# Kernel tuning notes

Hardware: AMD Instinct MI355X
Metric: run time of the kernel (lower is better)

Reference implementation:

```python
import jax, jax.numpy as jnp
import numpy as np

T, B, E, H = 2048, 2, 1024, 16
HD = E // H
EPS = 1e-5


def setup_inputs() -> dict:
    key = jax.random.key(0)
    k1, k2, k3 = jax.random.split(key, 3)
    bound_in = float(np.sqrt(6.0 / (3 * E + E)))   # xavier_uniform for [3E,E]
    bound_out = float(np.sqrt(6.0 / (E + E)))      # xavier_uniform for [E,E]
    return {
        "query": jax.random.normal(k1, (T, B, E), dtype=jnp.float32),
        "gamma": jnp.ones((E,), dtype=jnp.float32),
        "beta": jnp.zeros((E,), dtype=jnp.float32),
        "in_proj_weight": jax.random.uniform(k2, (3 * E, E), jnp.float32, -bound_in, bound_in),
        "out_proj_weight": jax.random.uniform(k3, (E, E), jnp.float32, -bound_out, bound_out),
    }


def reference(query, gamma, beta, in_proj_weight, out_proj_weight):
    # LayerNorm over channel dim
    mean = jnp.mean(query, axis=-1, keepdims=True)
    var = jnp.mean(jnp.square(query - mean), axis=-1, keepdims=True)
    ln = (query - mean) * jax.lax.rsqrt(var + EPS) * gamma + beta  # [T,B,E]

    # Fused QKV projection (no bias): qkv = ln @ W^T, W: [3E, E]
    qkv = jnp.einsum("tbe,fe->tbf", ln, in_proj_weight)  # [T,B,3E]
    q, k, v = jnp.split(qkv, 3, axis=-1)
    q = q.reshape(T, B, H, HD) * (HD ** -0.5)
    k = k.reshape(T, B, H, HD)
    v = v.reshape(T, B, H, HD)

    # Attention: scores [B,H,T,T]
    scores = jnp.einsum("tbhd,sbhd->bhts", q, k)
    attn = jax.nn.softmax(scores, axis=-1)
    ctx = jnp.einsum("bhts,sbhd->tbhd", attn, v).reshape(T, B, E)

    # Output projection + residual add (dropout prob = 0)
    out = jnp.einsum("tbe,fe->tbf", ctx, out_proj_weight)
    return query + out
```

## Files before the change

kernel.cpp:

```cpp
#include <hip/hip_runtime.h>
#include <hip/hip_bf16.h>
#include <math.h>

#define T_DIM 2048
#define B_DIM 2
#define E_DIM 1024
#define H_DIM 16
#define HD_DIM 64
#define M_DIM (T_DIM * B_DIM)
#define BH_DIM (B_DIM * H_DIM)

using bf16x8 = __attribute__((ext_vector_type(8))) __bf16;
using u16x8  = __attribute__((ext_vector_type(8))) unsigned short;
using u16x4  = __attribute__((ext_vector_type(4))) unsigned short;
using f32x4  = __attribute__((ext_vector_type(4))) float;

static __device__ __forceinline__ unsigned short f2bf(float f) {
  unsigned u = __builtin_bit_cast(unsigned, f);
  u += 0x7fff + ((u >> 16) & 1);
  return (unsigned short)(u >> 16);
}

__device__ __forceinline__ void gload_lds16(const void* g, void* l) {
  __builtin_amdgcn_global_load_lds(
      (const __attribute__((address_space(1))) unsigned int*)g,
      (__attribute__((address_space(3))) unsigned int*)l, 16, 0, 0);
}

__global__ __launch_bounds__(256) void cast_bf16_kernel(
    const float* __restrict__ in, unsigned short* __restrict__ out, int n4) {
  int i = blockIdx.x * 256 + threadIdx.x;
  if (i >= n4) return;
  float4 v = ((const float4*)in)[i];
  ushort4 o;
  o.x = f2bf(v.x); o.y = f2bf(v.y); o.z = f2bf(v.z); o.w = f2bf(v.w);
  ((ushort4*)out)[i] = o;
}

__global__ __launch_bounds__(256) void ln_kernel(
    const float* __restrict__ q, const float* __restrict__ gamma,
    const float* __restrict__ beta, unsigned short* __restrict__ out) {
  int row = blockIdx.x;
  int tid = threadIdx.x;
  const float4* qr = (const float4*)(q + (size_t)row * E_DIM);
  float4 x = qr[tid];
  float s  = x.x + x.y + x.z + x.w;
  float ss = x.x * x.x + x.y * x.y + x.z * x.z + x.w * x.w;
#pragma unroll
  for (int off = 32; off >= 1; off >>= 1) {
    s  += __shfl_xor(s, off, 64);
    ss += __shfl_xor(ss, off, 64);
  }
  __shared__ float red[8];
  int wid = tid >> 6, lane = tid & 63;
  if (lane == 0) { red[wid] = s; red[4 + wid] = ss; }
  __syncthreads();
  s  = red[0] + red[1] + red[2] + red[3];
  ss = red[4] + red[5] + red[6] + red[7];
  float mean = s * (1.0f / E_DIM);
  float var  = ss * (1.0f / E_DIM) - mean * mean;
  float rstd = rsqrtf(var + 1e-5f);
  float4 g4 = ((const float4*)gamma)[tid];
  float4 b4 = ((const float4*)beta)[tid];
  ushort4 o;
  o.x = f2bf((x.x - mean) * rstd * g4.x + b4.x);
  o.y = f2bf((x.y - mean) * rstd * g4.y + b4.y);
  o.z = f2bf((x.z - mean) * rstd * g4.z + b4.z);
  o.w = f2bf((x.w - mean) * rstd * g4.w + b4.w);
  ((ushort4*)(out + (size_t)row * E_DIM))[tid] = o;
}

template <int MODE>
__global__ __launch_bounds__(256) void gemm_bt_kernel(
    const unsigned short* __restrict__ A, const unsigned short* __restrict__ Bw,
    const float* __restrict__ resid, unsigned short* __restrict__ out_qkv,
    float* __restrict__ out_f, int Kv, int Nv) {
  __shared__ alignas(16) unsigned short lA[128 * 32];
  __shared__ alignas(16) unsigned short lB[128 * 32];
  int tid = threadIdx.x;
  int wid = tid >> 6, lane = tid & 63;
  int wm = wid >> 1, wn = wid & 1;
  int g = lane >> 4, lr = lane & 15;
  int m0 = blockIdx.y * 128, n0 = blockIdx.x * 128;
  f32x4 acc[4][4] = {};

  for (int k0 = 0; k0 < Kv; k0 += 32) {
#pragma unroll
    for (int c = 0; c < 2; ++c) {
      int f16 = c * 256 + tid;
      int row = f16 >> 2, col8 = (f16 & 3) << 3;
      gload_lds16(A  + (size_t)(m0 + row) * Kv + k0 + col8,
                  lA + (size_t)(c * 256 + wid * 64) * 8);
      gload_lds16(Bw + (size_t)(n0 + row) * Kv + k0 + col8,
                  lB + (size_t)(c * 256 + wid * 64) * 8);
    }
    __syncthreads();
    bf16x8 af[4], bfr[4];
#pragma unroll
    for (int r = 0; r < 4; ++r) {
      af[r]  = *(const bf16x8*)(lA + (wm * 64 + r * 16 + lr) * 32 + g * 8);
      bfr[r] = *(const bf16x8*)(lB + (wn * 64 + r * 16 + lr) * 32 + g * 8);
    }
#pragma unroll
    for (int mr = 0; mr < 4; ++mr)
#pragma unroll
      for (int nr = 0; nr < 4; ++nr)
        acc[mr][nr] = __builtin_amdgcn_mfma_f32_16x16x32_bf16(
            af[mr], bfr[nr], acc[mr][nr], 0, 0, 0);
    __syncthreads();
  }

#pragma unroll
  for (int mr = 0; mr < 4; ++mr) {
#pragma unroll
    for (int nr = 0; nr < 4; ++nr) {
#pragma unroll
      for (int r = 0; r < 4; ++r) {
        int grow = m0 + wm * 64 + mr * 16 + g * 4 + r;
        int gcol = n0 + wn * 64 + nr * 16 + lr;
        float v = acc[mr][nr][r];
        if (MODE == 0) {
          int which = gcol >> 10, rem = gcol & 1023;
          int h = rem >> 6, d = rem & 63;
          int t = grow >> 1, b = grow & 1;
          out_qkv[(size_t)which * (BH_DIM * T_DIM * HD_DIM) +
                  ((size_t)(b * H_DIM + h) * T_DIM + t) * HD_DIM + d] = f2bf(v);
        } else {
          size_t idx = (size_t)grow * Nv + gcol;
          out_f[idx] = resid[idx] + v;
        }
      }
    }
  }
}

__global__ __launch_bounds__(256) void transpose_v_kernel(
    const unsigned short* __restrict__ vb, unsigned short* __restrict__ vt) {
  __shared__ alignas(16) unsigned short tl[64 * 72];
  int tid = threadIdx.x;
  int bh = blockIdx.y, t0 = blockIdx.x * 64;
  const unsigned short* src = vb + ((size_t)bh * T_DIM + t0) * HD_DIM;
#pragma unroll
  for (int e = 0; e < 2; ++e) {
    int i8 = e * 256 + tid;
    int r = i8 >> 3;
    int c = (i8 & 7) * 8;
    int hsh = (r ^ (r >> 3)) & 7;
    bf16x8 v = *(const bf16x8*)(src + (size_t)r * HD_DIM + c);
    *(bf16x8*)(tl + r * 72 + (c ^ (hsh << 3))) = v;
  }
  __syncthreads();
  unsigned short* dst = vt + (size_t)bh * HD_DIM * T_DIM + t0;
#pragma unroll
  for (int e = 0; e < 2; ++e) {
    int i8 = e * 256 + tid;
    int d = i8 >> 3;
    int tc = (i8 & 7) * 8;
    u16x8 o;
#pragma unroll
    for (int j = 0; j < 8; ++j) {
      int p = tc + j;
      int r = ((p & 3) << 4) | (p >> 2);
      int hsh = (r ^ (r >> 3)) & 7;
      o[j] = tl[r * 72 + (d ^ (hsh << 3))];
    }
    *(u16x8*)(dst + (size_t)d * T_DIM + tc) = o;
  }
}

__global__ __launch_bounds__(256) void attn_kernel(
    const unsigned short* __restrict__ qb, const unsigned short* __restrict__ kb,
    const unsigned short* __restrict__ vt, unsigned short* __restrict__ ctx) {
  __shared__ alignas(16) unsigned short lK[3][64 * 64];
  __shared__ alignas(16) unsigned short lV[3][64 * 64];
  __shared__ alignas(16) unsigned short lP[4][32 * 72];
  int tid = threadIdx.x;
  int wid = tid >> 6, lane = tid & 63;
  int g = lane >> 4, lr = lane & 15;
  int bh = blockIdx.y;
  int b = bh >> 4, h = bh & 15;
  int qt = blockIdx.x;
  const size_t koff = (size_t)bh * T_DIM * HD_DIM;
  const size_t voff = (size_t)bh * HD_DIM * T_DIM;

  int srow = tid >> 3;
  int gch  = (tid & 7) ^ (srow & 7);
  const unsigned short* ks0 = kb + koff + (size_t)srow * HD_DIM + gch * 8;
  const unsigned short* vs0 = vt + voff + (size_t)srow * T_DIM + gch * 8;

#define STAGE_TILE(buf, kofs, vofs)                                            \
  do {                                                                         \
    gload_lds16(ks0 + (kofs),                 lK[buf] + wid * 512);            \
    gload_lds16(ks0 + (kofs) + 32 * HD_DIM,   lK[buf] + 2048 + wid * 512);     \
    gload_lds16(vs0 + (vofs),                 lV[buf] + wid * 512);            \
    gload_lds16(vs0 + (vofs) + (size_t)32 * T_DIM, lV[buf] + 2048 + wid * 512);\
  } while (0)

  bf16x8 qf[2][2];
  {
    const float QS = 0.125f * 1.44269504f;
#pragma unroll
    for (int qa = 0; qa < 2; ++qa) {
      int qrow = qt * 128 + wid * 32 + qa * 16 + lr;
#pragma unroll
      for (int ks = 0; ks < 2; ++ks) {
        bf16x8 raw = *(const bf16x8*)(qb + koff + (size_t)qrow * HD_DIM + ks * 32 + g * 8);
#pragma unroll
        for (int j = 0; j < 8; ++j) qf[qa][ks][j] = (__bf16)((float)raw[j] * QS);
      }
    }
  }

  bf16x8 onesf;
#pragma unroll
  for (int j = 0; j < 8; ++j) onesf[j] = (__bf16)1.0f;

  f32x4 accO[2][4] = {};
  f32x4 accS[2] = {};

  const int NT = T_DIM / 64;
  STAGE_TILE(0, 0, 0);

#define PROCESS(BUF, NBUF, TT, LAST)                                           \
  do {                                                                         \
    if (!(LAST)) {                                                             \
      size_t s1 = (size_t)((TT) + 1) * 64;                                     \
      STAGE_TILE(NBUF, s1 * HD_DIM, s1);                                       \
      asm volatile("s_waitcnt vmcnt(4)" ::: "memory");                         \
    } else {                                                                   \
      asm volatile("s_waitcnt vmcnt(0)" ::: "memory");                         \
    }                                                                          \
    __builtin_amdgcn_s_barrier();                                              \
    __builtin_amdgcn_sched_barrier(0);                                         \
    const unsigned short* Kc = lK[BUF];                                        \
    const unsigned short* Vc = lV[BUF];                                        \
    f32x4 s4[2][4];                                                            \
    __builtin_amdgcn_s_setprio(1);                                             \
    _Pragma("unroll")                                                          \
    for (int cf = 0; cf < 4; ++cf) {                                           \
      int row = cf * 16 + lr;                                                  \
      int sw = (row & 7) << 3;                                                 \
      bf16x8 k0 = *(const bf16x8*)(Kc + row * 64 + ((g * 8) ^ sw));            \
      bf16x8 k1 = *(const bf16x8*)(Kc + row * 64 + ((32 + g * 8) ^ sw));       \
      _Pragma("unroll")                                                        \
      for (int qa = 0; qa < 2; ++qa) {                                         \
        f32x4 s = {-8.0f, -8.0f, -8.0f, -8.0f};                                \
        s = __builtin_amdgcn_mfma_f32_16x16x32_bf16(qf[qa][0], k0, s, 0, 0, 0);\
        s = __builtin_amdgcn_mfma_f32_16x16x32_bf16(qf[qa][1], k1, s, 0, 0, 0);\
        s4[qa][cf] = s;                                                        \
      }                                                                        \
    }                                                                          \
    __builtin_amdgcn_s_setprio(0);                                             \
    _Pragma("unroll")                                                          \
    for (int qa = 0; qa < 2; ++qa)                                             \
      _Pragma("unroll")                                                        \
      for (int r = 0; r < 4; ++r) {                                            \
        u16x4 pk;                                                              \
        _Pragma("unroll")                                                      \
        for (int cf = 0; cf < 4; ++cf)                                         \
          pk[cf] = __builtin_bit_cast(unsigned short,                          \
                     (__bf16)__builtin_amdgcn_exp2f(s4[qa][cf][r]));           \
        *(u16x4*)(&lP[wid][(qa * 16 + g * 4 + r) * 72 + lr * 4]) = pk;         \
      }                                                                        \
    __builtin_amdgcn_s_setprio(1);                                             \
    _Pragma("unroll")                                                          \
    for (int ks = 0; ks < 2; ++ks) {                                           \
      bf16x8 pf[2];                                                            \
      _Pragma("unroll")                                                        \
      for (int qa = 0; qa < 2; ++qa) {                                         \
        pf[qa] = *(const bf16x8*)(&lP[wid][(qa * 16 + lr) * 72 + ks * 32 + g * 8]); \
        accS[qa] = __builtin_amdgcn_mfma_f32_16x16x32_bf16(pf[qa], onesf, accS[qa], 0, 0, 0); \
      }                                                                        \
      _Pragma("unroll")                                                        \
      for (int df = 0; df < 4; ++df) {                                         \
        int row = df * 16 + lr;                                                \
        int sw = (row & 7) << 3;                                               \
        bf16x8 vf = *(const bf16x8*)(Vc + row * 64 + ((ks * 32 + g * 8) ^ sw));\
        _Pragma("unroll")                                                      \
        for (int qa = 0; qa < 2; ++qa)                                         \
          accO[qa][df] = __builtin_amdgcn_mfma_f32_16x16x32_bf16(pf[qa], vf, accO[qa][df], 0, 0, 0); \
      }                                                                        \
    }                                                                          \
    __builtin_amdgcn_s_setprio(0);                                             \
  } while (0)

  for (int t3 = 0; t3 < 30; t3 += 3) {
    PROCESS(0, 1, t3 + 0, false);
    PROCESS(1, 2, t3 + 1, false);
    PROCESS(2, 0, t3 + 2, false);
  }
  PROCESS(0, 1, 30, false);
  PROCESS(1, 2, 31, true);
#undef PROCESS
#undef STAGE_TILE

#pragma unroll
  for (int qa = 0; qa < 2; ++qa) {
    float invl[4];
#pragma unroll
    for (int r = 0; r < 4; ++r) invl[r] = 1.0f / accS[qa][r];
#pragma unroll
    for (int df = 0; df < 4; ++df) {
#pragma unroll
      for (int r = 0; r < 4; ++r) {
        int t = qt * 128 + wid * 32 + qa * 16 + g * 4 + r;
        int col = h * HD_DIM + df * 16 + lr;
        float o = accO[qa][df][r] * invl[r];
        ctx[((size_t)t * B_DIM + b) * E_DIM + col] = f2bf(o);
      }
    }
  }
}

extern "C" void kernel_launch(void* const* d_in, const int* in_sizes, int n_in,
                              void* d_out, int out_size, void* d_ws, size_t ws_size,
                              hipStream_t stream) {
  const float* query = (const float*)d_in[0];
  const float* gamma = (const float*)d_in[1];
  const float* beta  = (const float*)d_in[2];
  const float* w_in  = (const float*)d_in[3];
  const float* w_out = (const float*)d_in[4];
  float* out = (float*)d_out;

  unsigned short* ws    = (unsigned short*)d_ws;
  unsigned short* ln    = ws;
  unsigned short* winb  = ln + (size_t)M_DIM * E_DIM;
  unsigned short* woutb = winb + (size_t)3 * E_DIM * E_DIM;
  unsigned short* qkv   = woutb + (size_t)E_DIM * E_DIM;

  unsigned short* qbuf = qkv;
  unsigned short* kbuf = qkv + (size_t)BH_DIM * T_DIM * HD_DIM;
  unsigned short* vbuf = kbuf + (size_t)BH_DIM * T_DIM * HD_DIM;
  unsigned short* vtb  = ln;
  unsigned short* ctx  = vbuf;

  cast_bf16_kernel<<<dim3(3072), dim3(256), 0, stream>>>(w_in, winb, 3 * E_DIM * E_DIM / 4);
  cast_bf16_kernel<<<dim3(1024), dim3(256), 0, stream>>>(w_out, woutb, E_DIM * E_DIM / 4);
  ln_kernel<<<dim3(M_DIM), dim3(256), 0, stream>>>(query, gamma, beta, ln);
  gemm_bt_kernel<0><<<dim3(3 * E_DIM / 128, M_DIM / 128), dim3(256), 0, stream>>>(
      ln, winb, nullptr, qkv, nullptr, E_DIM, 3 * E_DIM);
  transpose_v_kernel<<<dim3(T_DIM / 64, BH_DIM), dim3(256), 0, stream>>>(vbuf, vtb);
  attn_kernel<<<dim3(T_DIM / 128, BH_DIM), dim3(256), 0, stream>>>(qbuf, kbuf, vtb, ctx);
  gemm_bt_kernel<1><<<dim3(E_DIM / 128, M_DIM / 128), dim3(256), 0, stream>>>(
      ctx, woutb, query, nullptr, out, E_DIM, E_DIM);
}
```

Before: 137.7 us.

## Pre-pack K/V in MFMA fragment order and load attention operands directly to registers

The QKV GEMM epilogue now writes K straight into a fragment-packed layout, and the V transpose becomes a pack kernel that emits V in MFMA operand order. The attention kernel drops its LDS staging of K/V and loads fragments from global into registers, double-buffering K in registers. Blocks shrink to 128 threads over 64 query rows, and blocks are remapped so the heads sharing K/V land on the same XCD. The two weight casts are merged into one launch. This removes LDS traffic and barriers from the attention loop, at the cost of more global/L2 reads per block, since each block re-reads K/V for half as many queries, and higher register pressure.

```diff
diff --git a/kernel.cpp b/kernel.cpp
--- a/kernel.cpp
+++ b/kernel.cpp
@@ -27,14 +27,18 @@
       (__attribute__((address_space(3))) unsigned int*)l, 16, 0, 0);
 }
 
-__global__ __launch_bounds__(256) void cast_bf16_kernel(
-    const float* __restrict__ in, unsigned short* __restrict__ out, int n4) {
+__global__ __launch_bounds__(256) void cast2_kernel(
+    const float* __restrict__ in1, unsigned short* __restrict__ out1, int n1,
+    const float* __restrict__ in2, unsigned short* __restrict__ out2, int n2) {
   int i = blockIdx.x * 256 + threadIdx.x;
-  if (i >= n4) return;
-  float4 v = ((const float4*)in)[i];
+  const float* in; unsigned short* out; int idx;
+  if (i < n1) { in = in1; out = out1; idx = i; }
+  else if (i < n1 + n2) { in = in2; out = out2; idx = i - n1; }
+  else return;
+  float4 v = ((const float4*)in)[idx];
   ushort4 o;
   o.x = f2bf(v.x); o.y = f2bf(v.y); o.z = f2bf(v.z); o.w = f2bf(v.w);
-  ((ushort4*)out)[i] = o;
+  ((ushort4*)out)[idx] = o;
 }
 
 __global__ __launch_bounds__(256) void ln_kernel(
@@ -73,7 +77,8 @@
 template <int MODE>
 __global__ __launch_bounds__(256) void gemm_bt_kernel(
     const unsigned short* __restrict__ A, const unsigned short* __restrict__ Bw,
-    const float* __restrict__ resid, unsigned short* __restrict__ out_qkv,
+    const float* __restrict__ resid, unsigned short* __restrict__ out_q,
+    unsigned short* __restrict__ out_pk, unsigned short* __restrict__ out_v,
     float* __restrict__ out_f, int Kv, int Nv) {
   __shared__ alignas(16) unsigned short lA[128 * 32];
   __shared__ alignas(16) unsigned short lB[128 * 32];
@@ -123,8 +128,19 @@
           int which = gcol >> 10, rem = gcol & 1023;
           int h = rem >> 6, d = rem & 63;
           int t = grow >> 1, b = grow & 1;
-          out_qkv[(size_t)which * (BH_DIM * T_DIM * HD_DIM) +
-                  ((size_t)(b * H_DIM + h) * T_DIM + t) * HD_DIM + d] = f2bf(v);
+          size_t bh = (size_t)(b * H_DIM + h);
+          if (which == 0) {
+            out_q[(bh * T_DIM + t) * HD_DIM + d] = f2bf(v);
+          } else if (which == 1) {
+            int tile = t >> 6, trow = t & 63;
+            int cf = trow >> 4, ks = d >> 5;
+            int plane = ((d >> 3) & 3) * 16 + (trow & 15);
+            out_pk[bh * (32 * 8 * 512) +
+                   (size_t)((tile * 8) + cf * 2 + ks) * 512 + plane * 8 + (d & 7)]
+                = f2bf(v);
+          } else {
+            out_v[(bh * T_DIM + t) * HD_DIM + d] = f2bf(v);
+          }
         } else {
           size_t idx = (size_t)grow * Nv + gcol;
           out_f[idx] = resid[idx] + v;
@@ -134,74 +150,58 @@
   }
 }
 
-__global__ __launch_bounds__(256) void transpose_v_kernel(
-    const unsigned short* __restrict__ vb, unsigned short* __restrict__ vt) {
-  __shared__ alignas(16) unsigned short tl[64 * 72];
+__global__ __launch_bounds__(256) void pack_v_kernel(
+    const unsigned short* __restrict__ vb, unsigned short* __restrict__ pv) {
+  __shared__ alignas(16) unsigned short lV[64 * 72];
   int tid = threadIdx.x;
-  int bh = blockIdx.y, t0 = blockIdx.x * 64;
-  const unsigned short* src = vb + ((size_t)bh * T_DIM + t0) * HD_DIM;
+  int wid = tid >> 6, lane = tid & 63;
+  int tile = blockIdx.x, bh = blockIdx.y;
+  const unsigned short* src = vb + ((size_t)bh * T_DIM + tile * 64) * HD_DIM;
 #pragma unroll
   for (int e = 0; e < 2; ++e) {
     int i8 = e * 256 + tid;
-    int r = i8 >> 3;
-    int c = (i8 & 7) * 8;
-    int hsh = (r ^ (r >> 3)) & 7;
-    bf16x8 v = *(const bf16x8*)(src + (size_t)r * HD_DIM + c);
-    *(bf16x8*)(tl + r * 72 + (c ^ (hsh << 3))) = v;
+    int r = i8 >> 3, c = (i8 & 7) * 8;
+    *(bf16x8*)(lV + r * 72 + c) = *(const bf16x8*)(src + (size_t)r * HD_DIM + c);
   }
   __syncthreads();
-  unsigned short* dst = vt + (size_t)bh * HD_DIM * T_DIM + t0;
-#pragma unroll
-  for (int e = 0; e < 2; ++e) {
-    int i8 = e * 256 + tid;
-    int d = i8 >> 3;
-    int tc = (i8 & 7) * 8;
+  unsigned short* dst = pv + ((size_t)bh * 32 + tile) * (8 * 512);
+#pragma unroll
+  for (int q = 0; q < 2; ++q) {
+    int bv = wid * 2 + q;
+    int df = bv >> 1, ks = bv & 1;
     u16x8 o;
 #pragma unroll
     for (int j = 0; j < 8; ++j) {
-      int p = tc + j;
-      int r = ((p & 3) << 4) | (p >> 2);
-      int hsh = (r ^ (r >> 3)) & 7;
-      o[j] = tl[r * 72 + (d ^ (hsh << 3))];
-    }
-    *(u16x8*)(dst + (size_t)d * T_DIM + tc) = o;
-  }
-}
-
-__global__ __launch_bounds__(256) void attn_kernel(
-    const unsigned short* __restrict__ qb, const unsigned short* __restrict__ kb,
-    const unsigned short* __restrict__ vt, unsigned short* __restrict__ ctx) {
-  __shared__ alignas(16) unsigned short lK[3][64 * 64];
-  __shared__ alignas(16) unsigned short lV[3][64 * 64];
-  __shared__ alignas(16) unsigned short lP[4][32 * 72];
+      int p = ks * 32 + (lane >> 4) * 8 + j;
+      int tl = ((p & 3) << 4) | (p >> 2);
+      o[j] = lV[tl * 72 + df * 16 + (lane & 15)];
+    }
+    *(u16x8*)(dst + (size_t)bv * 512 + lane * 8) = o;
+  }
+}
+
+__global__ __launch_bounds__(128) void attn_kernel(
+    const unsigned short* __restrict__ qb, const unsigned short* __restrict__ pk,
+    const unsigned short* __restrict__ pv, unsigned short* __restrict__ ctx) {
+  __shared__ alignas(16) unsigned short lP[2][32 * 72];
   int tid = threadIdx.x;
   int wid = tid >> 6, lane = tid & 63;
   int g = lane >> 4, lr = lane & 15;
-  int bh = blockIdx.y;
+  int f = blockIdx.x;
+  int xcd = f & 7, k2 = f >> 3;
+  int bh = xcd + 8 * (k2 & 3);
+  int qt = k2 >> 2;
   int b = bh >> 4, h = bh & 15;
-  int qt = blockIdx.x;
   const size_t koff = (size_t)bh * T_DIM * HD_DIM;
-  const size_t voff = (size_t)bh * HD_DIM * T_DIM;
-
-  int srow = tid >> 3;
-  int gch  = (tid & 7) ^ (srow & 7);
-  const unsigned short* ks0 = kb + koff + (size_t)srow * HD_DIM + gch * 8;
-  const unsigned short* vs0 = vt + voff + (size_t)srow * T_DIM + gch * 8;
-
-#define STAGE_TILE(buf, kofs, vofs)                                            \
-  do {                                                                         \
-    gload_lds16(ks0 + (kofs),                 lK[buf] + wid * 512);            \
-    gload_lds16(ks0 + (kofs) + 32 * HD_DIM,   lK[buf] + 2048 + wid * 512);     \
-    gload_lds16(vs0 + (vofs),                 lV[buf] + wid * 512);            \
-    gload_lds16(vs0 + (vofs) + (size_t)32 * T_DIM, lV[buf] + 2048 + wid * 512);\
-  } while (0)
+  const unsigned short* pkb = pk + (size_t)bh * (32 * 8 * 512);
+  const unsigned short* pvb = pv + (size_t)bh * (32 * 8 * 512);
 
   bf16x8 qf[2][2];
   {
     const float QS = 0.125f * 1.44269504f;
 #pragma unroll
     for (int qa = 0; qa < 2; ++qa) {
-      int qrow = qt * 128 + wid * 32 + qa * 16 + lr;
+      int qrow = qt * 64 + wid * 32 + qa * 16 + lr;
 #pragma unroll
       for (int ks = 0; ks < 2; ++ks) {
         bf16x8 raw = *(const bf16x8*)(qb + koff + (size_t)qrow * HD_DIM + ks * 32 + g * 8);
@@ -218,49 +218,45 @@
   f32x4 accO[2][4] = {};
   f32x4 accS[2] = {};
 
-  const int NT = T_DIM / 64;
-  STAGE_TILE(0, 0, 0);
-
-#define PROCESS(BUF, NBUF, TT, LAST)                                           \
+  bf16x8 kfa[8], kfb[8];
+#pragma unroll
+  for (int bk = 0; bk < 8; ++bk)
+    kfa[bk] = *(const bf16x8*)(pkb + (size_t)bk * 512 + lane * 8);
+
+#define ITER(KC, KN, T, LAST)                                                  \
   do {                                                                         \
-    if (!(LAST)) {                                                             \
-      size_t s1 = (size_t)((TT) + 1) * 64;                                     \
-      STAGE_TILE(NBUF, s1 * HD_DIM, s1);                                       \
-      asm volatile("s_waitcnt vmcnt(4)" ::: "memory");                         \
-    } else {                                                                   \
-      asm volatile("s_waitcnt vmcnt(0)" ::: "memory");                         \
-    }                                                                          \
-    __builtin_amdgcn_s_barrier();                                              \
-    __builtin_amdgcn_sched_barrier(0);                                         \
-    const unsigned short* Kc = lK[BUF];                                        \
-    const unsigned short* Vc = lV[BUF];                                        \
+    bf16x8 vf[8];                                                              \
+    _Pragma("unroll")                                                          \
+    for (int bv = 0; bv < 8; ++bv)                                             \
+      vf[bv] = *(const bf16x8*)(pvb + ((size_t)(T) * 8 + bv) * 512 + lane * 8);\
     f32x4 s4[2][4];                                                            \
     __builtin_amdgcn_s_setprio(1);                                             \
     _Pragma("unroll")                                                          \
     for (int cf = 0; cf < 4; ++cf) {                                           \
-      int row = cf * 16 + lr;                                                  \
-      int sw = (row & 7) << 3;                                                 \
-      bf16x8 k0 = *(const bf16x8*)(Kc + row * 64 + ((g * 8) ^ sw));            \
-      bf16x8 k1 = *(const bf16x8*)(Kc + row * 64 + ((32 + g * 8) ^ sw));       \
       _Pragma("unroll")                                                        \
       for (int qa = 0; qa < 2; ++qa) {                                         \
         f32x4 s = {-8.0f, -8.0f, -8.0f, -8.0f};                                \
-        s = __builtin_amdgcn_mfma_f32_16x16x32_bf16(qf[qa][0], k0, s, 0, 0, 0);\
-        s = __builtin_amdgcn_mfma_f32_16x16x32_bf16(qf[qa][1], k1, s, 0, 0, 0);\
+        s = __builtin_amdgcn_mfma_f32_16x16x32_bf16(qf[qa][0], KC[cf * 2 + 0], s, 0, 0, 0); \
+        s = __builtin_amdgcn_mfma_f32_16x16x32_bf16(qf[qa][1], KC[cf * 2 + 1], s, 0, 0, 0); \
         s4[qa][cf] = s;                                                        \
       }                                                                        \
     }                                                                          \
     __builtin_amdgcn_s_setprio(0);                                             \
+    if (!(LAST)) {                                                             \
+      _Pragma("unroll")                                                        \
+      for (int bk = 0; bk < 8; ++bk)                                           \
+        KN[bk] = *(const bf16x8*)(pkb + ((size_t)((T) + 1) * 8 + bk) * 512 + lane * 8); \
+    }                                                                          \
     _Pragma("unroll")                                                          \
     for (int qa = 0; qa < 2; ++qa)                                             \
       _Pragma("unroll")                                                        \
       for (int r = 0; r < 4; ++r) {                                            \
-        u16x4 pk;                                                              \
+        u16x4 pkv;                                                             \
         _Pragma("unroll")                                                      \
         for (int cf = 0; cf < 4; ++cf)                                         \
-          pk[cf] = __builtin_bit_cast(unsigned short,                          \
-                     (__bf16)__builtin_amdgcn_exp2f(s4[qa][cf][r]));           \
-        *(u16x4*)(&lP[wid][(qa * 16 + g * 4 + r) * 72 + lr * 4]) = pk;         \
+          pkv[cf] = __builtin_bit_cast(unsigned short,                         \
+                      (__bf16)__builtin_amdgcn_exp2f(s4[qa][cf][r]));          \
+        *(u16x4*)(&lP[wid][(qa * 16 + g * 4 + r) * 72 + lr * 4]) = pkv;        \
       }                                                                        \
     __builtin_amdgcn_s_setprio(1);                                             \
     _Pragma("unroll")                                                          \
@@ -273,26 +269,19 @@
       }                                                                        \
       _Pragma("unroll")                                                        \
       for (int df = 0; df < 4; ++df) {                                         \
-        int row = df * 16 + lr;                                                \
-        int sw = (row & 7) << 3;                                               \
-        bf16x8 vf = *(const bf16x8*)(Vc + row * 64 + ((ks * 32 + g * 8) ^ sw));\
         _Pragma("unroll")                                                      \
         for (int qa = 0; qa < 2; ++qa)                                         \
-          accO[qa][df] = __builtin_amdgcn_mfma_f32_16x16x32_bf16(pf[qa], vf, accO[qa][df], 0, 0, 0); \
+          accO[qa][df] = __builtin_amdgcn_mfma_f32_16x16x32_bf16(pf[qa], vf[df * 2 + ks], accO[qa][df], 0, 0, 0); \
       }                                                                        \
     }                                                                          \
     __builtin_amdgcn_s_setprio(0);                                             \
   } while (0)
 
-  for (int t3 = 0; t3 < 30; t3 += 3) {
-    PROCESS(0, 1, t3 + 0, false);
-    PROCESS(1, 2, t3 + 1, false);
-    PROCESS(2, 0, t3 + 2, false);
-  }
-  PROCESS(0, 1, 30, false);
-  PROCESS(1, 2, 31, true);
-#undef PROCESS
-#undef STAGE_TILE
+  for (int t2 = 0; t2 < 32; t2 += 2) {
+    ITER(kfa, kfb, t2, false);
+    ITER(kfb, kfa, t2 + 1, t2 + 1 == 31);
+  }
+#undef ITER
 
 #pragma unroll
   for (int qa = 0; qa < 2; ++qa) {
@@ -303,7 +292,7 @@
     for (int df = 0; df < 4; ++df) {
 #pragma unroll
       for (int r = 0; r < 4; ++r) {
-        int t = qt * 128 + wid * 32 + qa * 16 + g * 4 + r;
+        int t = qt * 64 + wid * 32 + qa * 16 + g * 4 + r;
         int col = h * HD_DIM + df * 16 + lr;
         float o = accO[qa][df][r] * invl[r];
         ctx[((size_t)t * B_DIM + b) * E_DIM + col] = f2bf(o);
@@ -326,21 +315,19 @@
   unsigned short* ln    = ws;
   unsigned short* winb  = ln + (size_t)M_DIM * E_DIM;
   unsigned short* woutb = winb + (size_t)3 * E_DIM * E_DIM;
-  unsigned short* qkv   = woutb + (size_t)E_DIM * E_DIM;
-
-  unsigned short* qbuf = qkv;
-  unsigned short* kbuf = qkv + (size_t)BH_DIM * T_DIM * HD_DIM;
-  unsigned short* vbuf = kbuf + (size_t)BH_DIM * T_DIM * HD_DIM;
-  unsigned short* vtb  = ln;
-  unsigned short* ctx  = vbuf;
-
-  cast_bf16_kernel<<<dim3(3072), dim3(256), 0, stream>>>(w_in, winb, 3 * E_DIM * E_DIM / 4);
-  cast_bf16_kernel<<<dim3(1024), dim3(256), 0, stream>>>(w_out, woutb, E_DIM * E_DIM / 4);
+  unsigned short* qbuf  = woutb + (size_t)E_DIM * E_DIM;
+  unsigned short* vbuf  = qbuf + (size_t)BH_DIM * T_DIM * HD_DIM;
+  unsigned short* pk    = vbuf + (size_t)BH_DIM * T_DIM * HD_DIM;
+  unsigned short* pv    = ln;
+  unsigned short* ctx   = vbuf;
+
+  cast2_kernel<<<dim3(4096), dim3(256), 0, stream>>>(
+      w_in, winb, 3 * E_DIM * E_DIM / 4, w_out, woutb, E_DIM * E_DIM / 4);
   ln_kernel<<<dim3(M_DIM), dim3(256), 0, stream>>>(query, gamma, beta, ln);
   gemm_bt_kernel<0><<<dim3(3 * E_DIM / 128, M_DIM / 128), dim3(256), 0, stream>>>(
-      ln, winb, nullptr, qkv, nullptr, E_DIM, 3 * E_DIM);
-  transpose_v_kernel<<<dim3(T_DIM / 64, BH_DIM), dim3(256), 0, stream>>>(vbuf, vtb);
-  attn_kernel<<<dim3(T_DIM / 128, BH_DIM), dim3(256), 0, stream>>>(qbuf, kbuf, vtb, ctx);
+      ln, winb, nullptr, qbuf, pk, vbuf, nullptr, E_DIM, 3 * E_DIM);
+  pack_v_kernel<<<dim3(T_DIM / 64, BH_DIM), dim3(256), 0, stream>>>(vbuf, pv);
+  attn_kernel<<<dim3(1024), dim3(128), 0, stream>>>(qbuf, pk, pv, ctx);
   gemm_bt_kernel<1><<<dim3(E_DIM / 128, M_DIM / 128), dim3(256), 0, stream>>>(
-      ctx, woutb, query, nullptr, out, E_DIM, E_DIM);
-}
+      ctx, woutb, query, nullptr, nullptr, nullptr, out, E_DIM, E_DIM);
+}
```

Result: slower. 143.7 us (+4.3%).
